# Kernel optimization log

Measured on AMD Instinct MI355X. Metric: run time of the kernel, lower is better.

## Reference

```python
import jax, jax.numpy as jnp
import numpy as np

N_VAR, N_CSTR, E, D = 100_000, 50_000, 1_000_000, 64
BN_EPS = 1e-5


def setup_inputs() -> dict:
    key = jax.random.key(0)
    ks = jax.random.split(key, 12)
    s = 0.05
    return {
        "var_feats": jax.random.normal(ks[0], (N_VAR, D), jnp.float32),
        "cstr_feats": jax.random.normal(ks[1], (N_CSTR, D), jnp.float32),
        "edge_src": jax.random.randint(ks[2], (E,), 0, N_CSTR),  # cstr indices
        "edge_dst": jax.random.randint(ks[3], (E,), 0, N_VAR),   # var indices
        "edge_attr": jax.random.normal(ks[4], (E,), jnp.float32),
        # BatchNorm affine params
        "node_bn_gamma": jnp.ones((D,), jnp.float32),
        "node_bn_beta": jnp.zeros((D,), jnp.float32),
        "cstr_bn_gamma": jnp.ones((D,), jnp.float32),
        "cstr_bn_beta": jnp.zeros((D,), jnp.float32),
        # node_gnn = GraphConv(in=(cstr_dim, node_dim), out=node_dim, aggr='mean')
        "node_rel_w": s * jax.random.normal(ks[5], (D, D), jnp.float32),
        "node_rel_b": s * jax.random.normal(ks[6], (D,), jnp.float32),
        "node_root_w": s * jax.random.normal(ks[7], (D, D), jnp.float32),
        # cstr_gnn = GraphConv(in=(node_dim, cstr_dim), out=cstr_dim, aggr='mean')
        "cstr_rel_w": s * jax.random.normal(ks[8], (D, D), jnp.float32),
        "cstr_rel_b": s * jax.random.normal(ks[9], (D,), jnp.float32),
        "cstr_root_w": s * jax.random.normal(ks[10], (D, D), jnp.float32),
    }


def _batch_norm(x, gamma, beta):
    # training-mode BatchNorm1d over the node axis (biased variance)
    m = jnp.mean(x, axis=0)
    v = jnp.var(x, axis=0)
    return (x - m) * jax.lax.rsqrt(v + BN_EPS) * gamma + beta


def _graph_conv(x_src, x_dst, src, dst, ew, w_rel, b_rel, w_root):
    # message: edge_weight * x_src[src], scatter-mean onto destinations
    msg = x_src[src] * ew                                   # [E, D]
    n_dst = x_dst.shape[0]
    ssum = jax.ops.segment_sum(msg, dst, num_segments=n_dst)          # [n_dst, D]
    cnt = jax.ops.segment_sum(jnp.ones((src.shape[0],), x_dst.dtype), dst,
                              num_segments=n_dst)                     # [n_dst]
    agg = ssum / jnp.maximum(cnt, 1.0)[:, None]
    return agg @ w_rel.T + b_rel + x_dst @ w_root.T


def reference(var_feats, cstr_feats, edge_src, edge_dst, edge_attr,
              node_bn_gamma, node_bn_beta, cstr_bn_gamma, cstr_bn_beta,
              node_rel_w, node_rel_b, node_root_w,
              cstr_rel_w, cstr_rel_b, cstr_root_w):
    x_node = _batch_norm(var_feats, node_bn_gamma, node_bn_beta)
    x_cstr = _batch_norm(cstr_feats, cstr_bn_gamma, cstr_bn_beta)
    ew = edge_attr[:, None]                                  # [E, 1]
    # node_gnn: source = cstr, dst = node (edge_index as given)
    x_node_ = _graph_conv(x_cstr, x_node, edge_src, edge_dst, ew,
                          node_rel_w, node_rel_b, node_root_w)
    # cstr_gnn: flipped edge_index -> source = node, dst = cstr
    x_cstr_ = _graph_conv(x_node, x_cstr, edge_dst, edge_src, ew,
                          cstr_rel_w, cstr_rel_b, cstr_root_w)
    x_node_ = jax.nn.relu(x_node_ + x_node)  # residual=True
    x_cstr_ = jax.nn.relu(x_cstr_ + x_cstr)
    return x_node_, x_cstr_
```

## Files before the change

### kernel.cpp

```cpp
#include <hip/hip_runtime.h>

#define N_VAR   100000
#define N_CSTR  50000
#define NEDGE   1000000
#define DIM     64

#define NBK_N 782
#define NBK_C 391
#define NBK_T 1173
#define NCHUNK 245

#define OFF_STATS  0
#define OFF_BHIST  256
#define OFF_AB     1536
#define OFF_GBN    1792
#define OFF_GBC    2592
#define OFF_GCN    3008
#define OFF_GCC    3808
#define OFF_OFF_N  4224
#define OFF_OFF_C  104228
#define OFF_XCB    154232
#define OFF_XNB    1754232
#define OFF_ENT_N  4954232
#define OFF_ENT_C  6954232
#define WS_ZERO_N  1536

__global__ __launch_bounds__(256) void bn_stats_k(const float* __restrict__ x, int n,
                                                  float* __restrict__ stats) {
  int c = threadIdx.x & 63;
  int rg = threadIdx.x >> 6;
  float s = 0.f, q = 0.f;
  for (int r = blockIdx.x * 4 + rg; r < n; r += gridDim.x * 4) {
    float v = x[r * DIM + c];
    s += v;
    q += v * v;
  }
  __shared__ float sb[256], qb[256];
  sb[threadIdx.x] = s;
  qb[threadIdx.x] = q;
  __syncthreads();
  if (rg == 0) {
    s = sb[c] + sb[c + 64] + sb[c + 128] + sb[c + 192];
    q = qb[c] + qb[c + 64] + qb[c + 128] + qb[c + 192];
    atomicAdd(&stats[c], s);
    atomicAdd(&stats[64 + c], q);
  }
}

__global__ void bn_finalize_k(const float* __restrict__ stats,
                              const float* __restrict__ gn, const float* __restrict__ bn,
                              const float* __restrict__ gc, const float* __restrict__ bc,
                              float* __restrict__ ab) {
  int t = threadIdx.x;
  int c = t & 63;
  bool isC = t >= 64;
  const float* st = stats + (isC ? 128 : 0);
  float n = isC ? (float)N_CSTR : (float)N_VAR;
  float mean = st[c] / n;
  float var = st[64 + c] / n - mean * mean;
  float g = isC ? gc[c] : gn[c];
  float be = isC ? bc[c] : bn[c];
  float a = g * rsqrtf(var + 1e-5f);
  float b = be - mean * a;
  float* o = ab + (isC ? 128 : 0);
  o[c] = a;
  o[64 + c] = b;
}

__device__ __forceinline__ unsigned short f2bf(float f) {
  unsigned u = __float_as_uint(f);
  return (unsigned short)((u + 0x7FFFu + ((u >> 16) & 1u)) >> 16);
}

__global__ __launch_bounds__(256) void cvt_k(const float4* __restrict__ src4,
                                             const float* __restrict__ ab,
                                             ushort4* __restrict__ dst, int n4) {
  int i4 = blockIdx.x * 256 + threadIdx.x;
  if (i4 >= n4) return;
  float4 v = src4[i4];
  int c0 = (i4 << 2) & 63;
  ushort4 o;
  o.x = f2bf(fmaf(v.x, ab[c0 + 0], ab[64 + c0 + 0]));
  o.y = f2bf(fmaf(v.y, ab[c0 + 1], ab[64 + c0 + 1]));
  o.z = f2bf(fmaf(v.z, ab[c0 + 2], ab[64 + c0 + 2]));
  o.w = f2bf(fmaf(v.w, ab[c0 + 3], ab[64 + c0 + 3]));
  dst[i4] = o;
}

__global__ __launch_bounds__(256) void bhist_k(const int4* __restrict__ es4,
                                               const int4* __restrict__ ed4,
                                               int* __restrict__ ws) {
  __shared__ int h[1280];
  for (int i = threadIdx.x; i < 1280; i += 256) h[i] = 0;
  __syncthreads();
  int stride = gridDim.x * 256;
  for (int i4 = blockIdx.x * 256 + threadIdx.x; i4 < NEDGE / 4; i4 += stride) {
    int4 d = ed4[i4];
    int4 s = es4[i4];
    atomicAdd(&h[d.x >> 7], 1);
    atomicAdd(&h[d.y >> 7], 1);
    atomicAdd(&h[d.z >> 7], 1);
    atomicAdd(&h[d.w >> 7], 1);
    atomicAdd(&h[NBK_N + (s.x >> 7)], 1);
    atomicAdd(&h[NBK_N + (s.y >> 7)], 1);
    atomicAdd(&h[NBK_N + (s.z >> 7)], 1);
    atomicAdd(&h[NBK_N + (s.w >> 7)], 1);
  }
  __syncthreads();
  int* gh = ws + OFF_BHIST;
  for (int i = threadIdx.x; i < NBK_T; i += 256)
    if (h[i]) atomicAdd(&gh[i], h[i]);
}

__global__ __launch_bounds__(256) void bscan_k(int* __restrict__ ws) {
  __shared__ int sb[256];
  int t = threadIdx.x;
#pragma unroll
  for (int seg = 0; seg < 2; ++seg) {
    int nbk = seg ? NBK_C : NBK_N;
    const int* h = ws + OFF_BHIST + (seg ? NBK_N : 0);
    int* gb = ws + (seg ? OFF_GBC : OFF_GBN);
    int* gc = ws + (seg ? OFF_GCC : OFF_GCN);
    int base = t * 4;
    int c[4];
    int s0 = 0;
#pragma unroll
    for (int j = 0; j < 4; ++j) {
      c[j] = (base + j < nbk) ? h[base + j] : 0;
      s0 += c[j];
    }
    sb[t] = s0;
    __syncthreads();
    for (int d = 1; d < 256; d <<= 1) {
      int v = (t >= d) ? sb[t - d] : 0;
      __syncthreads();
      sb[t] += v;
      __syncthreads();
    }
    int ex = sb[t] - s0;
#pragma unroll
    for (int j = 0; j < 4; ++j) {
      if (base + j < nbk) {
        gb[base + j] = ex;
        gc[base + j] = ex;
      }
      ex += c[j];
    }
    if (t == 255) gb[nbk] = sb[255];
    __syncthreads();
  }
  if (t == 0) {
    ws[OFF_OFF_N + N_VAR] = NEDGE;
    ws[OFF_OFF_C + N_CSTR] = NEDGE;
  }
}

__global__ __launch_bounds__(256) void passA_k(const int4* __restrict__ es4,
                                               const int4* __restrict__ ed4,
                                               const float4* __restrict__ ea4,
                                               int* __restrict__ ws) {
  __shared__ int cntL[1024];
  __shared__ int runoffL[1024];
  __shared__ int gblL[1024];
  __shared__ int2 dataL[4096];
  __shared__ unsigned short bidL[4096];
  __shared__ int sbL[256];
  int side = (blockIdx.x >= NCHUNK);
  int chunk = side ? blockIdx.x - NCHUNK : blockIdx.x;
  int nbk = side ? NBK_C : NBK_N;
  int* gcur = ws + (side ? OFF_GCC : OFF_GCN);
  int2* ent = (int2*)(ws + (side ? OFF_ENT_C : OFF_ENT_N));
  int t = threadIdx.x;
  for (int i = t; i < 1024; i += 256) cntL[i] = 0;
  __syncthreads();
  int e0 = chunk * 4096;
  int base4 = chunk * 1024 + t * 4;
  int pk[16];
  int2 pay[16];
#pragma unroll
  for (int j = 0; j < 4; ++j) {
    int i4 = base4 + j;
    if (i4 < NEDGE / 4) {
      int4 sv = es4[i4];
      int4 dv = ed4[i4];
      float4 wv = ea4[i4];
      int ss[4] = {sv.x, sv.y, sv.z, sv.w};
      int dd[4] = {dv.x, dv.y, dv.z, dv.w};
      float ww[4] = {wv.x, wv.y, wv.z, wv.w};
#pragma unroll
      for (int k = 0; k < 4; ++k) {
        int s = ss[k], d = dd[k];
        int b = side ? (s >> 7) : (d >> 7);
        int pl = side ? (d | ((s & 127) << 17)) : (s | ((d & 127) << 17));
        int rank = atomicAdd(&cntL[b], 1);
        pk[j * 4 + k] = b * 4096 + rank;
        pay[j * 4 + k] = make_int2(pl, __float_as_int(ww[k]));
      }
    } else {
#pragma unroll
      for (int k = 0; k < 4; ++k) pk[j * 4 + k] = -1;
    }
  }
  __syncthreads();
  int base = t * 4;
  int c[4];
  int s0 = 0;
#pragma unroll
  for (int j = 0; j < 4; ++j) {
    c[j] = cntL[base + j];
    s0 += c[j];
  }
  sbL[t] = s0;
  __syncthreads();
  for (int d = 1; d < 256; d <<= 1) {
    int v = (t >= d) ? sbL[t - d] : 0;
    __syncthreads();
    sbL[t] += v;
    __syncthreads();
  }
  int ex = sbL[t] - s0;
#pragma unroll
  for (int j = 0; j < 4; ++j) {
    runoffL[base + j] = ex;
    ex += c[j];
  }
  __syncthreads();
  for (int b = t; b < nbk; b += 256) {
    int cc = cntL[b];
    gblL[b] = cc ? atomicAdd(&gcur[b], cc) : 0;
  }
  __syncthreads();
#pragma unroll
  for (int j = 0; j < 16; ++j) {
    if (pk[j] >= 0) {
      int b = pk[j] >> 12;
      int slot = runoffL[b] + (pk[j] & 4095);
      dataL[slot] = pay[j];
      bidL[slot] = (unsigned short)b;
    }
  }
  __syncthreads();
  int chunkN = min(4096, NEDGE - e0);
  for (int i = t; i < chunkN; i += 256) {
    int b = bidL[i];
    ent[gblL[b] + (i - runoffL[b])] = dataL[i];
  }
}

__global__ __launch_bounds__(256) void sort_k(int* __restrict__ ws) {
  __shared__ int2 data[4096];
  __shared__ int hcnt[128], hrank[128];
  __shared__ int sb[128];
  int x = blockIdx.x;
  int side = (x >= NBK_N);
  int bk = side ? x - NBK_N : x;
  const int* gbase = ws + (side ? OFF_GBC : OFF_GBN);
  int2* ent = (int2*)(ws + (side ? OFF_ENT_C : OFF_ENT_N));
  int* off = ws + (side ? OFF_OFF_C : OFF_OFF_N);
  int n = side ? N_CSTR : N_VAR;
  int t = threadIdx.x;
  int beg = gbase[bk], end = gbase[bk + 1];
  int cnt = end - beg;
  if (t < 128) hcnt[t] = 0;
  __syncthreads();
  for (int i = t; i < cnt; i += 256) {
    int2 e = ent[beg + i];
    data[i] = e;
    atomicAdd(&hcnt[(e.x >> 17) & 127], 1);
  }
  __syncthreads();
  if (t < 128) sb[t] = hcnt[t];
  __syncthreads();
  for (int d = 1; d < 128; d <<= 1) {
    int v = 0;
    if (t < 128 && t >= d) v = sb[t - d];
    __syncthreads();
    if (t < 128) sb[t] += v;
    __syncthreads();
  }
  if (t < 128) {
    int ex = sb[t] - hcnt[t];
    hrank[t] = ex;
    int r = bk * 128 + t;
    if (r < n) off[r] = beg + ex;
  }
  __syncthreads();
  for (int i = t; i < cnt; i += 256) {
    int2 e = data[i];
    int dl = (e.x >> 17) & 127;
    int pos = atomicAdd(&hrank[dl], 1);
    ent[beg + pos] = make_int2(e.x & 0x1FFFF, e.y);
  }
}

__global__ __launch_bounds__(256) void gather_k(
    const unsigned short* __restrict__ tab, const int2* __restrict__ ent,
    const int* __restrict__ off, float* __restrict__ agg, int n) {
  int lane = threadIdx.x & 63;
  int r = __builtin_amdgcn_readfirstlane((blockIdx.x * blockDim.x + threadIdx.x) >> 6);
  if (r >= n) return;
  int beg = off[r], end = off[r + 1];
  float acc0 = 0.f, acc1 = 0.f;
  int e = beg;
#define BF(hv) __uint_as_float(((unsigned)(hv)) << 16)
  if (e < end && (e & 1)) {
    int2 p = ent[e];
    acc0 = fmaf(BF(tab[p.x * DIM + lane]), __int_as_float(p.y), acc0);
    ++e;
  }
  for (; e + 8 <= end; e += 8) {
    int4 p0 = *reinterpret_cast<const int4*>(&ent[e]);
    int4 p1 = *reinterpret_cast<const int4*>(&ent[e + 2]);
    int4 p2 = *reinterpret_cast<const int4*>(&ent[e + 4]);
    int4 p3 = *reinterpret_cast<const int4*>(&ent[e + 6]);
    float v0 = BF(tab[p0.x * DIM + lane]);
    float v1 = BF(tab[p0.z * DIM + lane]);
    float v2 = BF(tab[p1.x * DIM + lane]);
    float v3 = BF(tab[p1.z * DIM + lane]);
    float v4 = BF(tab[p2.x * DIM + lane]);
    float v5 = BF(tab[p2.z * DIM + lane]);
    float v6 = BF(tab[p3.x * DIM + lane]);
    float v7 = BF(tab[p3.z * DIM + lane]);
    acc0 = fmaf(v0, __int_as_float(p0.y), acc0);
    acc1 = fmaf(v1, __int_as_float(p0.w), acc1);
    acc0 = fmaf(v2, __int_as_float(p1.y), acc0);
    acc1 = fmaf(v3, __int_as_float(p1.w), acc1);
    acc0 = fmaf(v4, __int_as_float(p2.y), acc0);
    acc1 = fmaf(v5, __int_as_float(p2.w), acc1);
    acc0 = fmaf(v6, __int_as_float(p3.y), acc0);
    acc1 = fmaf(v7, __int_as_float(p3.w), acc1);
  }
  for (; e + 2 <= end; e += 2) {
    int4 p = *reinterpret_cast<const int4*>(&ent[e]);
    acc0 = fmaf(BF(tab[p.x * DIM + lane]), __int_as_float(p.y), acc0);
    acc1 = fmaf(BF(tab[p.z * DIM + lane]), __int_as_float(p.w), acc1);
  }
  if (e < end) {
    int2 p = ent[e];
    acc0 = fmaf(BF(tab[p.x * DIM + lane]), __int_as_float(p.y), acc0);
  }
#undef BF
  agg[(long)r * DIM + lane] = (acc0 + acc1) / fmaxf((float)(end - beg), 1.f);
}

__global__ __launch_bounds__(256) void out_k(
    const float* __restrict__ raw, const float* __restrict__ ab,
    const float* __restrict__ w_rel, const float* __restrict__ b_rel,
    const float* __restrict__ w_root, float* __restrict__ io, int n) {
  int lane = threadIdx.x & 63;
  float a = ab[lane], b = ab[64 + lane];
  float brel = b_rel[lane];
  float4 wr[16], wo[16];
#pragma unroll
  for (int i = 0; i < 16; ++i) {
    wr[i] = reinterpret_cast<const float4*>(w_rel + lane * DIM)[i];
    wo[i] = reinterpret_cast<const float4*>(w_root + lane * DIM)[i];
  }
  int wave = (blockIdx.x * blockDim.x + threadIdx.x) >> 6;
  int nw = (gridDim.x * blockDim.x) >> 6;
  for (int r = wave; r < n; r += nw) {
    float av = io[r * DIM + lane];
    float xv = fmaf(raw[r * DIM + lane], a, b);
    int avi = __float_as_int(av);
    int xvi = __float_as_int(xv);
    float acc0 = 0.f, acc1 = 0.f, acc2 = 0.f, acc3 = 0.f;
#pragma unroll
    for (int i = 0; i < 16; ++i) {
      acc0 = fmaf(__int_as_float(__builtin_amdgcn_readlane(avi, 4 * i + 0)), wr[i].x, acc0);
      acc1 = fmaf(__int_as_float(__builtin_amdgcn_readlane(avi, 4 * i + 1)), wr[i].y, acc1);
      acc2 = fmaf(__int_as_float(__builtin_amdgcn_readlane(avi, 4 * i + 2)), wr[i].z, acc2);
      acc3 = fmaf(__int_as_float(__builtin_amdgcn_readlane(avi, 4 * i + 3)), wr[i].w, acc3);
      acc0 = fmaf(__int_as_float(__builtin_amdgcn_readlane(xvi, 4 * i + 0)), wo[i].x, acc0);
      acc1 = fmaf(__int_as_float(__builtin_amdgcn_readlane(xvi, 4 * i + 1)), wo[i].y, acc1);
      acc2 = fmaf(__int_as_float(__builtin_amdgcn_readlane(xvi, 4 * i + 2)), wo[i].z, acc2);
      acc3 = fmaf(__int_as_float(__builtin_amdgcn_readlane(xvi, 4 * i + 3)), wo[i].w, acc3);
    }
    io[r * DIM + lane] = fmaxf((acc0 + acc1) + (acc2 + acc3) + brel + xv, 0.f);
  }
}

extern "C" void kernel_launch(void* const* d_in, const int* in_sizes, int n_in,
                              void* d_out, int out_size, void* d_ws, size_t ws_size,
                              hipStream_t stream) {
  const float* vf = (const float*)d_in[0];
  const float* cf = (const float*)d_in[1];
  const int* es = (const int*)d_in[2];
  const int* ed = (const int*)d_in[3];
  const float* ea = (const float*)d_in[4];
  const float* gn = (const float*)d_in[5];
  const float* bn = (const float*)d_in[6];
  const float* gc = (const float*)d_in[7];
  const float* bc = (const float*)d_in[8];
  const float* n_rel_w = (const float*)d_in[9];
  const float* n_rel_b = (const float*)d_in[10];
  const float* n_root_w = (const float*)d_in[11];
  const float* c_rel_w = (const float*)d_in[12];
  const float* c_rel_b = (const float*)d_in[13];
  const float* c_root_w = (const float*)d_in[14];
  float* out = (float*)d_out;
  int* wsi = (int*)d_ws;
  float* wsf = (float*)d_ws;

  float* stats = wsf + OFF_STATS;
  float* ab = wsf + OFF_AB;
  ushort4* xcb = (ushort4*)(wsi + OFF_XCB);
  ushort4* xnb = (ushort4*)(wsi + OFF_XNB);
  const unsigned short* xcb_s = (const unsigned short*)(wsi + OFF_XCB);
  const unsigned short* xnb_s = (const unsigned short*)(wsi + OFF_XNB);
  const int2* ent_n = (const int2*)(wsi + OFF_ENT_N);
  const int2* ent_c = (const int2*)(wsi + OFF_ENT_C);

  float* agg_node = out;
  float* agg_cstr = out + (long)N_VAR * DIM;

  hipMemsetAsync(d_ws, 0, (size_t)WS_ZERO_N * sizeof(int), stream);

  bn_stats_k<<<512, 256, 0, stream>>>(vf, N_VAR, stats);
  bn_stats_k<<<512, 256, 0, stream>>>(cf, N_CSTR, stats + 128);
  bn_finalize_k<<<1, 128, 0, stream>>>(stats, gn, bn, gc, bc, ab);

  cvt_k<<<(N_CSTR * DIM / 4 + 255) / 256, 256, 0, stream>>>((const float4*)cf, ab + 128,
                                                            xcb, N_CSTR * DIM / 4);
  cvt_k<<<(N_VAR * DIM / 4 + 255) / 256, 256, 0, stream>>>((const float4*)vf, ab,
                                                           xnb, N_VAR * DIM / 4);

  bhist_k<<<128, 256, 0, stream>>>((const int4*)es, (const int4*)ed, wsi);
  bscan_k<<<1, 256, 0, stream>>>(wsi);
  passA_k<<<2 * NCHUNK, 256, 0, stream>>>((const int4*)es, (const int4*)ed,
                                          (const float4*)ea, wsi);
  sort_k<<<NBK_T, 256, 0, stream>>>(wsi);

  gather_k<<<(N_VAR + 3) / 4, 256, 0, stream>>>(xcb_s, ent_n, wsi + OFF_OFF_N,
                                                agg_node, N_VAR);
  gather_k<<<(N_CSTR + 3) / 4, 256, 0, stream>>>(xnb_s, ent_c, wsi + OFF_OFF_C,
                                                 agg_cstr, N_CSTR);

  out_k<<<1024, 256, 0, stream>>>(vf, ab, n_rel_w, n_rel_b, n_root_w, agg_node, N_VAR);
  out_k<<<512, 256, 0, stream>>>(cf, ab + 128, c_rel_w, c_rel_b, c_root_w, agg_cstr,
                                 N_CSTR);
}
```

Baseline: 375.6 us.

## Compute output linear layers with bf16 MFMA instead of readlane FMAs

Replaces the per-row readlane-based fp32 dot-product output kernel with an MFMA kernel. Each wave processes 16-row tiles, concatenating the aggregated and normalized root features into a K=128 bf16 operand. Weights are preloaded as bf16 fragments in registers. This removes the heavy scalar readlane and VALU cost but lowers the precision of the linear layers to bf16, and it uses a strided, uncoalesced epilogue store. Rows beyond a multiple of 16 are not handled, which is fine for the given sizes.

```diff
diff --git a/kernel.cpp b/kernel.cpp
--- a/kernel.cpp
+++ b/kernel.cpp
@@ -24,6 +24,9 @@
 #define OFF_ENT_N  4954232
 #define OFF_ENT_C  6954232
 #define WS_ZERO_N  1536
+
+typedef __attribute__((ext_vector_type(8))) short bf16x8;
+typedef __attribute__((ext_vector_type(4))) float f32x4;
 
 __global__ __launch_bounds__(256) void bn_stats_k(const float* __restrict__ x, int n,
                                                   float* __restrict__ stats) {
@@ -343,39 +346,70 @@
   agg[(long)r * DIM + lane] = (acc0 + acc1) / fmaxf((float)(end - beg), 1.f);
 }
 
-__global__ __launch_bounds__(256) void out_k(
+__global__ __launch_bounds__(256) void out_mfma_k(
     const float* __restrict__ raw, const float* __restrict__ ab,
     const float* __restrict__ w_rel, const float* __restrict__ b_rel,
     const float* __restrict__ w_root, float* __restrict__ io, int n) {
-  int lane = threadIdx.x & 63;
-  float a = ab[lane], b = ab[64 + lane];
-  float brel = b_rel[lane];
-  float4 wr[16], wo[16];
-#pragma unroll
-  for (int i = 0; i < 16; ++i) {
-    wr[i] = reinterpret_cast<const float4*>(w_rel + lane * DIM)[i];
-    wo[i] = reinterpret_cast<const float4*>(w_root + lane * DIM)[i];
-  }
-  int wave = (blockIdx.x * blockDim.x + threadIdx.x) >> 6;
-  int nw = (gridDim.x * blockDim.x) >> 6;
-  for (int r = wave; r < n; r += nw) {
-    float av = io[r * DIM + lane];
-    float xv = fmaf(raw[r * DIM + lane], a, b);
-    int avi = __float_as_int(av);
-    int xvi = __float_as_int(xv);
-    float acc0 = 0.f, acc1 = 0.f, acc2 = 0.f, acc3 = 0.f;
-#pragma unroll
-    for (int i = 0; i < 16; ++i) {
-      acc0 = fmaf(__int_as_float(__builtin_amdgcn_readlane(avi, 4 * i + 0)), wr[i].x, acc0);
-      acc1 = fmaf(__int_as_float(__builtin_amdgcn_readlane(avi, 4 * i + 1)), wr[i].y, acc1);
-      acc2 = fmaf(__int_as_float(__builtin_amdgcn_readlane(avi, 4 * i + 2)), wr[i].z, acc2);
-      acc3 = fmaf(__int_as_float(__builtin_amdgcn_readlane(avi, 4 * i + 3)), wr[i].w, acc3);
-      acc0 = fmaf(__int_as_float(__builtin_amdgcn_readlane(xvi, 4 * i + 0)), wo[i].x, acc0);
-      acc1 = fmaf(__int_as_float(__builtin_amdgcn_readlane(xvi, 4 * i + 1)), wo[i].y, acc1);
-      acc2 = fmaf(__int_as_float(__builtin_amdgcn_readlane(xvi, 4 * i + 2)), wo[i].z, acc2);
-      acc3 = fmaf(__int_as_float(__builtin_amdgcn_readlane(xvi, 4 * i + 3)), wo[i].w, acc3);
-    }
-    io[r * DIM + lane] = fmaxf((acc0 + acc1) + (acc2 + acc3) + brel + xv, 0.f);
+  int t = threadIdx.x;
+  int lane = t & 63, wv = t >> 6;
+  int quad = lane >> 4, l16 = lane & 15;
+
+  bf16x8 bfrag[4][4];
+#pragma unroll
+  for (int nt = 0; nt < 4; ++nt) {
+    int c = nt * 16 + l16;
+#pragma unroll
+    for (int kc = 0; kc < 4; ++kc) {
+      int bk = kc * 32 + quad * 8;
+      const float* wsrc = (bk < 64) ? (w_rel + c * 64 + bk) : (w_root + c * 64 + bk - 64);
+      bf16x8 f;
+#pragma unroll
+      for (int j = 0; j < 8; ++j) f[j] = (short)f2bf(wsrc[j]);
+      bfrag[nt][kc] = f;
+    }
+  }
+  float av0[8], bv0[8], av1[8], bv1[8];
+#pragma unroll
+  for (int j = 0; j < 8; ++j) {
+    av0[j] = ab[quad * 8 + j];
+    bv0[j] = ab[64 + quad * 8 + j];
+    av1[j] = ab[32 + quad * 8 + j];
+    bv1[j] = ab[96 + quad * 8 + j];
+  }
+
+  int tiles = n >> 4;
+  for (int tile = blockIdx.x * 4 + wv; tile < tiles; tile += gridDim.x * 4) {
+    int r0 = tile << 4;
+    const float* aggr = io + (long)(r0 + l16) * DIM;
+    const float* rawr = raw + (long)(r0 + l16) * DIM;
+    bf16x8 a0, a1, a2, a3;
+#pragma unroll
+    for (int j = 0; j < 8; ++j) {
+      a0[j] = (short)f2bf(aggr[quad * 8 + j]);
+      a1[j] = (short)f2bf(aggr[32 + quad * 8 + j]);
+      a2[j] = (short)f2bf(fmaf(rawr[quad * 8 + j], av0[j], bv0[j]));
+      a3[j] = (short)f2bf(fmaf(rawr[32 + quad * 8 + j], av1[j], bv1[j]));
+    }
+    f32x4 acc[4];
+#pragma unroll
+    for (int nt = 0; nt < 4; ++nt) {
+      acc[nt] = (f32x4){0.f, 0.f, 0.f, 0.f};
+      acc[nt] = __builtin_amdgcn_mfma_f32_16x16x32_bf16(a0, bfrag[nt][0], acc[nt], 0, 0, 0);
+      acc[nt] = __builtin_amdgcn_mfma_f32_16x16x32_bf16(a1, bfrag[nt][1], acc[nt], 0, 0, 0);
+      acc[nt] = __builtin_amdgcn_mfma_f32_16x16x32_bf16(a2, bfrag[nt][2], acc[nt], 0, 0, 0);
+      acc[nt] = __builtin_amdgcn_mfma_f32_16x16x32_bf16(a3, bfrag[nt][3], acc[nt], 0, 0, 0);
+    }
+#pragma unroll
+    for (int nt = 0; nt < 4; ++nt) {
+      int c = nt * 16 + l16;
+      float aC = ab[c], bC = ab[64 + c], brC = b_rel[c];
+#pragma unroll
+      for (int reg = 0; reg < 4; ++reg) {
+        int r = r0 + quad * 4 + reg;
+        float xv = fmaf(raw[(long)r * DIM + c], aC, bC);
+        io[(long)r * DIM + c] = fmaxf(acc[nt][reg] + brC + xv, 0.f);
+      }
+    }
   }
 }
 
@@ -435,7 +469,8 @@
   gather_k<<<(N_CSTR + 3) / 4, 256, 0, stream>>>(xnb_s, ent_c, wsi + OFF_OFF_C,
                                                  agg_cstr, N_CSTR);
 
-  out_k<<<1024, 256, 0, stream>>>(vf, ab, n_rel_w, n_rel_b, n_root_w, agg_node, N_VAR);
-  out_k<<<512, 256, 0, stream>>>(cf, ab + 128, c_rel_w, c_rel_b, c_root_w, agg_cstr,
-                                 N_CSTR);
-}
+  out_mfma_k<<<640, 256, 0, stream>>>(vf, ab, n_rel_w, n_rel_b, n_root_w,
+                                      agg_node, N_VAR);
+  out_mfma_k<<<320, 256, 0, stream>>>(cf, ab + 128, c_rel_w, c_rel_b, c_root_w,
+                                      agg_cstr, N_CSTR);
+}
```

After: 333.8 us. 1.13x faster.
